# Kernel optimization log

Measured on AMD Instinct MI355X. Metric: run time of the kernel, lower is better.

Reference implementation:

```python
import jax, jax.numpy as jnp
import numpy as np

MAX_WARPING_WINDOW = None  # matches init kwarg (None => full window, no masking)


def _pairwise_euclidean(x, y):
    # x: (B, F, Tx), y: (B, F, Ty) -> (B, Tx, Ty)
    # ||x_t - y_s||_2 computed via the expanded quadratic form (one GEMM instead
    # of materializing the (B, F, Tx, Ty) difference tensor like the torch code).
    x2 = jnp.sum(x * x, axis=1)                      # (B, Tx)
    y2 = jnp.sum(y * y, axis=1)                      # (B, Ty)
    xy = jnp.einsum('bft,bfs->bts', x, y)            # (B, Tx, Ty)
    d2 = jnp.maximum(x2[:, :, None] + y2[:, None, :] - 2.0 * xy, 0.0)
    return jnp.sqrt(d2)


def _dtw(cost):
    # cost: (B, Tx, Ty). Classic DTW DP:
    #   dtw[i, j] = cost[i-1, j-1] + min(dtw[i-1, j], dtw[i, j-1], dtw[i-1, j-1])
    # outer scan over rows i, inner scan over columns j (carries dtw[i, j-1]).
    B, Tx, Ty = cost.shape
    dt = cost.dtype
    INF = jnp.array(jnp.inf, dt)
    cost_t = jnp.transpose(cost, (1, 2, 0))          # (Tx, Ty, B)

    def row_step(carry, cost_row):
        prev_row, left = carry                       # prev_row: (Ty, B) = dtw[i-1, 1:], left: (B,) = dtw[i-1, 0]
        prev_shift = jnp.concatenate([left[None, :], prev_row[:-1]], axis=0)  # dtw[i-1, j-1]
        a = jnp.minimum(prev_row, prev_shift)        # min(dtw[i-1, j], dtw[i-1, j-1])

        def col_step(cur_left, ac):
            a_j, c_j = ac                            # each (B,)
            cur = c_j + jnp.minimum(a_j, cur_left)   # cur_left = dtw[i, j-1]
            return cur, cur

        _, cur_row = jax.lax.scan(col_step, jnp.full((B,), INF, dt), (a, cost_row))
        return (cur_row, jnp.full((B,), INF, dt)), None

    # row 0 of the DP: dtw[0, 0] = 0, dtw[0, j>0] = inf
    init = (jnp.full((Ty, B), INF, dt), jnp.zeros((B,), dt))
    (last_row, _), _ = jax.lax.scan(row_step, init, cost_t)
    return last_row[-1]                              # dtw[Tx, Ty], shape (B,)


def setup_inputs() -> dict:
    key = jax.random.key(0)
    kx, ky = jax.random.split(key)
    B, F, T = 128, 128, 512
    x = jax.random.normal(kx, (B, F, T), dtype=jnp.float32)
    y = jax.random.normal(ky, (B, F, T), dtype=jnp.float32)
    return {"x": x, "y": y}


def reference(x, y):
    cost = _pairwise_euclidean(x, y)                 # (B, Tx, Ty)
    if MAX_WARPING_WINDOW is not None:
        Tx, Ty = cost.shape[1], cost.shape[2]
        p = jnp.arange(Tx)[:, None]
        q = jnp.arange(Ty)[None, :]
        cost = jnp.where(jnp.abs(p - q) <= MAX_WARPING_WINDOW, cost, jnp.inf)
    return _dtw(cost)
```

## Files before the change

kernel.cpp:

```cpp
#include <hip/hip_runtime.h>
#include <stdint.h>

#define B_ 128
#define F_ 128
#define T_ 512
#define TS 64
#define DIAG_N 1024

#define BIGV 1e30f

typedef __attribute__((ext_vector_type(8))) short     bf16x8;
typedef __attribute__((ext_vector_type(4))) float     f32x4;
typedef __attribute__((ext_vector_type(2))) float     f32x2;

static __device__ __forceinline__ unsigned short f32_to_bf16(float f) {
    union { float f; uint32_t u; } v; v.f = f;
    const uint32_t u = v.u + 0x7fffu + ((v.u >> 16) & 1u);
    return (unsigned short)(u >> 16);
}

static __device__ __forceinline__ float wave_shr1(float src, float fill) {
    const int r = __builtin_amdgcn_update_dpp(
        __builtin_bit_cast(int, fill), __builtin_bit_cast(int, src),
        0x138, 0xf, 0xf, false);
    return __builtin_bit_cast(float, r);
}
static __device__ __forceinline__ float wave_shl1(float src, float fill) {
    const int r = __builtin_amdgcn_update_dpp(
        __builtin_bit_cast(int, fill), __builtin_bit_cast(int, src),
        0x130, 0xf, 0xf, false);
    return __builtin_bit_cast(float, r);
}

__global__ __launch_bounds__(256) void dtw_prep_kernel(
    const float* __restrict__ x, const float* __restrict__ y,
    unsigned short* __restrict__ xt, unsigned short* __restrict__ yt,
    float* __restrict__ nx, float* __restrict__ ny)
{
    const int tch = blockIdx.x;
    const int b   = blockIdx.y;
    const int z   = blockIdx.z;
    const int tid = threadIdx.x;
    const int t0  = tch * 64;

    const float* src      = (z == 0 ? x : y) + (size_t)b * F_ * T_;
    unsigned short* dst   = (z == 0 ? xt : yt) + (size_t)b * T_ * F_;
    float* nd             = (z == 0 ? nx : ny) + (size_t)b * T_;

    __shared__ float S[F_][65];

    const int fr = tid >> 4;
    const int q  = (tid & 15) * 4;
#pragma unroll
    for (int p = 0; p < 8; ++p) {
        const int f = p * 16 + fr;
        const float4 v = *(const float4*)(src + (size_t)f * T_ + t0 + q);
        S[f][q] = v.x; S[f][q + 1] = v.y; S[f][q + 2] = v.z; S[f][q + 3] = v.w;
    }
    __syncthreads();

    if (tid < 64) {
        float s = 0.f;
#pragma unroll
        for (int f = 0; f < F_; ++f) { const float v = S[f][tid]; s = fmaf(v, v, s); }
        nd[t0 + tid] = s;
    }

    const int tl = tid >> 2;
    const int fb = (tid & 3) * 32;
    uint32_t pk[16];
#pragma unroll
    for (int e = 0; e < 16; ++e) {
        const uint32_t lo = f32_to_bf16(S[fb + 2 * e][tl]);
        const uint32_t hi = f32_to_bf16(S[fb + 2 * e + 1][tl]);
        pk[e] = lo | (hi << 16);
    }
    uint32_t* o = (uint32_t*)(dst + (size_t)(t0 + tl) * F_ + fb);
#pragma unroll
    for (int e = 0; e < 16; e += 4)
        *(uint4*)(o + e) = make_uint4(pk[e], pk[e + 1], pk[e + 2], pk[e + 3]);
}

__global__ __launch_bounds__(256) void dtw_cost_kernel(
    const unsigned short* __restrict__ xt, const unsigned short* __restrict__ yt,
    const float* __restrict__ nx, const float* __restrict__ ny,
    unsigned char* __restrict__ costD, int b0)
{
    const int tj  = blockIdx.x;
    const int ti  = blockIdx.y;
    const int bl  = blockIdx.z;
    const int b   = b0 + bl;
    const int tid = threadIdx.x;
    const int gi0 = ti * TS;
    const int gj0 = tj * TS;

    const int w    = tid >> 6;
    const int lane = tid & 63;
    const int l15  = lane & 15;
    const int hi   = lane >> 4;

    __shared__ __align__(16) char smem[16384];
    unsigned short* Ys = (unsigned short*)smem;

    {
        const int l16 = tid & 15;
#pragma unroll
        for (int p = 0; p < 4; ++p) {
            const int row = p * 16 + (tid >> 4);
            const uint4 vy = *(const uint4*)(yt + ((size_t)b * T_ + gj0 + row) * F_ + l16 * 8);
            const int byt = (row * 256 + l16 * 16) ^ ((row & 7) << 4);
            *(uint4*)((char*)Ys + byt) = vy;
        }
    }

    const unsigned short* xb = xt + ((size_t)b * T_ + gi0 + 16 * w + l15) * F_ + hi * 8;
    const bf16x8 A0 = *(const bf16x8*)(xb);
    const bf16x8 A1 = *(const bf16x8*)(xb + 32);
    const bf16x8 A2 = *(const bf16x8*)(xb + 64);
    const bf16x8 A3 = *(const bf16x8*)(xb + 96);

    const float4 x2r = *(const float4*)(nx + (size_t)b * T_ + gi0 + 16 * w + 4 * hi);
    float y2c[4];
#pragma unroll
    for (int nt = 0; nt < 4; ++nt)
        y2c[nt] = ny[(size_t)b * T_ + gj0 + nt * 16 + l15];
    const float x2v[4] = {x2r.x, x2r.y, x2r.z, x2r.w};

    __syncthreads();

    f32x4 acc[4] = {};
#pragma unroll
    for (int kb = 0; kb < 4; ++kb) {
        const int koff = kb * 64 + hi * 16;
        const bf16x8 a = (kb == 0) ? A0 : (kb == 1) ? A1 : (kb == 2) ? A2 : A3;
#pragma unroll
        for (int nt = 0; nt < 4; ++nt) {
            const int col = nt * 16 + l15;
            const bf16x8 bb = *(const bf16x8*)((const char*)Ys +
                               ((col * 256 + koff) ^ ((col & 7) << 4)));
            acc[nt] = __builtin_amdgcn_mfma_f32_16x16x32_bf16(a, bb, acc[nt], 0, 0, 0);
        }
    }

    __syncthreads();
    unsigned short* Ts = (unsigned short*)smem;
#pragma unroll
    for (int nt = 0; nt < 4; ++nt) {
        const int col = nt * 16 + l15;
#pragma unroll
        for (int r = 0; r < 4; ++r) {
            const int row = 16 * w + hi * 4 + r;
            const float c = sqrtf(fmaxf(x2v[r] + y2c[nt] - 2.f * acc[nt][r], 0.f));
            const _Float16 hv = (_Float16)c;
            Ts[row * 67 + col] = *(const unsigned short*)&hv;
        }
    }
    __syncthreads();

    unsigned char* outD = costD + (size_t)bl * (DIAG_N * (size_t)T_);
    const int tbase = gi0 + gj0;
#pragma unroll
    for (int q = 0; q < 16; ++q) {
        const int g = q * 4 + w;
        const int d = (lane <= g) ? g : g + 64;
        const _Float16 hval = *(const _Float16*)&Ts[(d - lane) * 67 + lane];
        const float cf = (float)hval;
        const int pk = __builtin_amdgcn_cvt_pk_fp8_f32(cf, cf, 0, false);
        outD[(size_t)(tbase + d) * T_ + gj0 + lane] = (unsigned char)pk;
    }
}

__global__ __launch_bounds__(128, 1) void dtw_dp_bidi(
    const unsigned char* __restrict__ costD, float* __restrict__ out, int b0)
{
    const int bl  = blockIdx.x;
    const int tid = threadIdx.x;
    const int w   = tid >> 6;
    const int L   = tid & 63;
    const unsigned char* gbase = costD + (size_t)bl * (DIAG_N * (size_t)T_) + 16 * L;

    __shared__ __align__(16) unsigned char ringF[32][T_];
    __shared__ __align__(16) unsigned char ringB[32][T_];
    __shared__ __align__(16) float bb2[T_];
    __shared__ __align__(16) float bb3[T_];

    float va0 = BIGV, va1 = BIGV, va2 = BIGV, va3 = BIGV,
          va4 = BIGV, va5 = BIGV, va6 = BIGV, va7 = BIGV;
    float vb0 = BIGV, vb1 = BIGV, vb2 = BIGV, vb3 = BIGV,
          vb4 = BIGV, vb5 = BIGV, vb6 = BIGV, vb7 = BIGV;
    float s2c;
    uint2 ca0, ca1, ca2, ca3, ca4, ca5, ca6, ca7;
    uint2 cb0, cb1, cb2, cb3, cb4, cb5, cb6, cb7;

#define GLDP(RING, row, slot)                                               \
    __builtin_amdgcn_global_load_lds(                                       \
        (const __attribute__((address_space(1))) void*)(gbase + (size_t)(row) * T_), \
        (__attribute__((address_space(3))) void*)(&RING[slot][0]), 16, 0, 0)

#define GLD4F(blk) do {                                                     \
    const int r0_ = (blk) * 8, s0_ = ((blk) & 3) * 8;                       \
    GLDP(ringF, r0_ + 0, s0_ + 0); GLDP(ringF, r0_ + 2, s0_ + 2);           \
    GLDP(ringF, r0_ + 4, s0_ + 4); GLDP(ringF, r0_ + 6, s0_ + 6);           \
} while (0)

#define GLD4B(blk) do {                                                     \
    const int m0_ = 1015 - (blk) * 8, s0_ = ((blk) & 3) * 8;                \
    GLDP(ringB, m0_ + 0, s0_ + 0); GLDP(ringB, m0_ + 2, s0_ + 2);           \
    GLDP(ringB, m0_ + 4, s0_ + 4); GLDP(ringB, m0_ + 6, s0_ + 6);           \
} while (0)

#define WAITV(n)                                                            \
    do { asm volatile("s_waitcnt vmcnt(" #n ")" ::: "memory");              \
         __builtin_amdgcn_sched_barrier(0); } while (0)

#define SB __builtin_amdgcn_sched_barrier(0)

#define RL8(BK, blk) do {                                                   \
    const unsigned char* rp_ = &ringF[((blk) & 3) * 8][8 * L];              \
    BK##0 = *(const uint2*)(rp_ + 0 * T_);                                  \
    BK##1 = *(const uint2*)(rp_ + 1 * T_);                                  \
    BK##2 = *(const uint2*)(rp_ + 2 * T_);                                  \
    BK##3 = *(const uint2*)(rp_ + 3 * T_);                                  \
    BK##4 = *(const uint2*)(rp_ + 4 * T_);                                  \
    BK##5 = *(const uint2*)(rp_ + 5 * T_);                                  \
    BK##6 = *(const uint2*)(rp_ + 6 * T_);                                  \
    BK##7 = *(const uint2*)(rp_ + 7 * T_);                                  \
} while (0)

#define RL8R(BK, blk) do {                                                  \
    const unsigned char* rp_ = &ringB[((blk) & 3) * 8][8 * L];              \
    BK##0 = *(const uint2*)(rp_ + 7 * T_);                                  \
    BK##1 = *(const uint2*)(rp_ + 6 * T_);                                  \
    BK##2 = *(const uint2*)(rp_ + 5 * T_);                                  \
    BK##3 = *(const uint2*)(rp_ + 4 * T_);                                  \
    BK##4 = *(const uint2*)(rp_ + 3 * T_);                                  \
    BK##5 = *(const uint2*)(rp_ + 2 * T_);                                  \
    BK##6 = *(const uint2*)(rp_ + 1 * T_);                                  \
    BK##7 = *(const uint2*)(rp_ + 0 * T_);                                  \
} while (0)

#define CVT8(Hv)                                                            \
    const f32x2 c01 = __builtin_amdgcn_cvt_pk_f32_fp8((int)Hv.x, false);    \
    const f32x2 c23 = __builtin_amdgcn_cvt_pk_f32_fp8((int)Hv.x, true);     \
    const f32x2 c45 = __builtin_amdgcn_cvt_pk_f32_fp8((int)Hv.y, false);    \
    const f32x2 c67 = __builtin_amdgcn_cvt_pk_f32_fp8((int)Hv.y, true)

#define STEPF_A(Hv) do {                                                    \
    const float s1 = wave_shr1(va7, BIGV);                                  \
    CVT8(Hv);                                                               \
    const float n0 = c01[0] + fminf(fminf(va0, s1),  s2c);                  \
    const float n1 = c01[1] + fminf(fminf(va1, va0), vb0);                  \
    const float n2 = c23[0] + fminf(fminf(va2, va1), vb1);                  \
    const float n3 = c23[1] + fminf(fminf(va3, va2), vb2);                  \
    const float n4 = c45[0] + fminf(fminf(va4, va3), vb3);                  \
    const float n5 = c45[1] + fminf(fminf(va5, va4), vb4);                  \
    const float n6 = c67[0] + fminf(fminf(va6, va5), vb5);                  \
    const float n7 = c67[1] + fminf(fminf(va7, va6), vb6);                  \
    s2c = s1;                                                               \
    vb0 = n0; vb1 = n1; vb2 = n2; vb3 = n3;                                 \
    vb4 = n4; vb5 = n5; vb6 = n6; vb7 = n7;                                 \
} while (0)

#define STEPF_B(Hv) do {                                                    \
    const float s1 = wave_shr1(vb7, BIGV);                                  \
    CVT8(Hv);                                                               \
    const float n0 = c01[0] + fminf(fminf(vb0, s1),  s2c);                  \
    const float n1 = c01[1] + fminf(fminf(vb1, vb0), va0);                  \
    const float n2 = c23[0] + fminf(fminf(vb2, vb1), va1);                  \
    const float n3 = c23[1] + fminf(fminf(vb3, vb2), va2);                  \
    const float n4 = c45[0] + fminf(fminf(vb4, vb3), va3);                  \
    const float n5 = c45[1] + fminf(fminf(vb5, vb4), va4);                  \
    const float n6 = c67[0] + fminf(fminf(vb6, vb5), va5);                  \
    const float n7 = c67[1] + fminf(fminf(vb7, vb6), va6);                  \
    s2c = s1;                                                               \
    va0 = n0; va1 = n1; va2 = n2; va3 = n3;                                 \
    va4 = n4; va5 = n5; va6 = n6; va7 = n7;                                 \
} while (0)

#define STEPB_A(Hv) do {                                                    \
    const float s1 = wave_shl1(va0, BIGV);                                  \
    CVT8(Hv);                                                               \
    const float n7 = c67[1] + fminf(fminf(va7, s1),  s2c);                  \
    const float n6 = c67[0] + fminf(fminf(va6, va7), vb7);                  \
    const float n5 = c45[1] + fminf(fminf(va5, va6), vb6);                  \
    const float n4 = c45[0] + fminf(fminf(va4, va5), vb5);                  \
    const float n3 = c23[1] + fminf(fminf(va3, va4), vb4);                  \
    const float n2 = c23[0] + fminf(fminf(va2, va3), vb3);                  \
    const float n1 = c01[1] + fminf(fminf(va1, va2), vb2);                  \
    const float n0 = c01[0] + fminf(fminf(va0, va1), vb1);                  \
    s2c = s1;                                                               \
    vb0 = n0; vb1 = n1; vb2 = n2; vb3 = n3;                                 \
    vb4 = n4; vb5 = n5; vb6 = n6; vb7 = n7;                                 \
} while (0)

#define STEPB_B(Hv) do {                                                    \
    const float s1 = wave_shl1(vb0, BIGV);                                  \
    CVT8(Hv);                                                               \
    const float n7 = c67[1] + fminf(fminf(vb7, s1),  s2c);                  \
    const float n6 = c67[0] + fminf(fminf(vb6, vb7), va7);                  \
    const float n5 = c45[1] + fminf(fminf(vb5, vb6), va6);                  \
    const float n4 = c45[0] + fminf(fminf(vb4, vb5), va5);                  \
    const float n3 = c23[1] + fminf(fminf(vb3, vb4), va4);                  \
    const float n2 = c23[0] + fminf(fminf(vb2, vb3), va3);                  \
    const float n1 = c01[1] + fminf(fminf(vb1, vb2), va2);                  \
    const float n0 = c01[0] + fminf(fminf(vb0, vb1), va1);                  \
    s2c = s1;                                                               \
    va0 = n0; va1 = n1; va2 = n2; va3 = n3;                                 \
    va4 = n4; va5 = n5; va6 = n6; va7 = n7;                                 \
} while (0)

#define STEPF8(BK)                                                          \
    STEPF_A(BK##0); STEPF_B(BK##1); STEPF_A(BK##2); STEPF_B(BK##3);         \
    STEPF_A(BK##4); STEPF_B(BK##5); STEPF_A(BK##6); STEPF_B(BK##7)
#define STEPB8(BK)                                                          \
    STEPB_A(BK##0); STEPB_B(BK##1); STEPB_A(BK##2); STEPB_B(BK##3);         \
    STEPB_A(BK##4); STEPB_B(BK##5); STEPB_A(BK##6); STEPB_B(BK##7)

    if (w == 0) {
        s2c = (L == 0) ? 0.f : BIGV;
        GLD4F(0); GLD4F(1); GLD4F(2); GLD4F(3);
        WAITV(12); RL8(ca, 0); SB;
        int k = 0;
#pragma unroll 1
        for (int it = 0; it < 30; ++it) {
            WAITV(8); RL8(cb, k + 1); SB; STEPF8(ca); SB; GLD4F(k + 4); SB;
            WAITV(8); RL8(ca, k + 2); SB; STEPF8(cb); SB; GLD4F(k + 5); SB;
            k += 2;
        }
        WAITV(8); RL8(cb, 61); SB; STEPF8(ca); SB;
        WAITV(4); RL8(ca, 62); SB; STEPF8(cb); SB;
        WAITV(0); RL8(cb, 63); SB; STEPF8(ca); SB;
        STEPF8(cb);
    } else {
        s2c = (L == 63) ? 0.f : BIGV;
        GLD4B(0); GLD4B(1); GLD4B(2); GLD4B(3);
        WAITV(12); RL8R(ca, 0); SB;
        int k = 0;
#pragma unroll 1
        for (int it = 0; it < 30; ++it) {
            WAITV(8); RL8R(cb, k + 1); SB; STEPB8(ca); SB; GLD4B(k + 4); SB;
            WAITV(8); RL8R(ca, k + 2); SB; STEPB8(cb); SB; GLD4B(k + 5); SB;
            k += 2;
        }
        WAITV(8); RL8R(cb, 61); SB; STEPB8(ca); SB;
        WAITV(4); RL8R(ca, 62); SB; STEPB8(cb); SB;
        WAITV(0); RL8R(cb, 63); SB; STEPB8(ca); SB;
        STEPB_A(cb0); STEPB_B(cb1); STEPB_A(cb2); STEPB_B(cb3);
        STEPB_A(cb4); STEPB_B(cb5); STEPB_A(cb6);
        *(float4*)&bb2[8 * L]     = make_float4(vb0, vb1, vb2, vb3);
        *(float4*)&bb2[8 * L + 4] = make_float4(vb4, vb5, vb6, vb7);
        *(float4*)&bb3[8 * L]     = make_float4(va0, va1, va2, va3);
        *(float4*)&bb3[8 * L + 4] = make_float4(va4, va5, va6, va7);
    }

    __syncthreads();

    if (w == 0) {
        const float4 p0 = *(const float4*)&bb2[8 * L];
        const float4 p1 = *(const float4*)&bb2[8 * L + 4];
        const float4 q0 = *(const float4*)&bb3[8 * L];
        const float4 q1 = *(const float4*)&bb3[8 * L + 4];
        const float b2[8] = {p0.x, p0.y, p0.z, p0.w, p1.x, p1.y, p1.z, p1.w};
        const float b3[8] = {q0.x, q0.y, q0.z, q0.w, q1.x, q1.y, q1.z, q1.w};
        const float F511[8] = {va0, va1, va2, va3, va4, va5, va6, va7};
        const float F510[8] = {vb0, vb1, vb2, vb3, vb4, vb5, vb6, vb7};
        float b2s[8], b3s[8];
#pragma unroll
        for (int kk = 0; kk < 7; ++kk) { b2s[kk] = b2[kk + 1]; b3s[kk] = b3[kk + 1]; }
        b2s[7] = wave_shl1(b2[0], BIGV);
        b3s[7] = wave_shl1(b3[0], BIGV);
        float m = BIGV;
#pragma unroll
        for (int kk = 0; kk < 8; ++kk) {
            const float t1 = F511[kk] + fminf(fminf(b2[kk], b2s[kk]), b3s[kk]);
            const float t2 = F510[kk] + b2s[kk];
            m = fminf(m, fminf(t1, t2));
        }
#pragma unroll
        for (int off = 1; off < 64; off <<= 1)
            m = fminf(m, __shfl_xor(m, off));
        if (L == 0) out[b0 + bl] = m;
    }

#undef GLDP
#undef GLD4F
#undef GLD4B
#undef WAITV
#undef SB
#undef RL8
#undef RL8R
#undef CVT8
#undef STEPF_A
#undef STEPF_B
#undef STEPB_A
#undef STEPB_B
#undef STEPF8
#undef STEPB8
}

extern "C" void kernel_launch(void* const* d_in, const int* in_sizes, int n_in,
                              void* d_out, int out_size, void* d_ws, size_t ws_size,
                              hipStream_t stream)
{
    const float* x = (const float*)d_in[0];
    const float* y = (const float*)d_in[1];
    float* out = (float*)d_out;

    unsigned short* xt = (unsigned short*)d_ws;
    unsigned short* yt = xt + (size_t)B_ * T_ * F_;
    float* nx = (float*)(yt + (size_t)B_ * T_ * F_);
    float* ny = nx + (size_t)B_ * T_;
    unsigned char* costD = (unsigned char*)(ny + (size_t)B_ * T_);
    const size_t head = (size_t)(costD - (unsigned char*)d_ws);

    const size_t perb = (size_t)DIAG_N * T_;
    int Bg = 8;
    for (int g = 128; g >= 8; g >>= 1)
        if (ws_size >= head + perb * (size_t)g) { Bg = g; break; }

    hipLaunchKernelGGL(dtw_prep_kernel, dim3(T_ / 64, B_, 2), dim3(256), 0, stream,
                       x, y, xt, yt, nx, ny);

    for (int b0 = 0; b0 < B_; b0 += Bg) {
        dim3 gc(T_ / TS, T_ / TS, Bg);
        hipLaunchKernelGGL(dtw_cost_kernel, gc, dim3(256), 0, stream,
                           xt, yt, nx, ny, costD, b0);
        hipLaunchKernelGGL(dtw_dp_bidi, dim3(Bg), dim3(128), 0, stream,
                           costD, out, b0);
    }
}
```

Baseline: 97.03 us.

## Interleave two independent batch DTW recurrences per wave in the DP kernel

```diff
diff --git a/kernel.cpp b/kernel.cpp
--- a/kernel.cpp
+++ b/kernel.cpp
@@ -170,43 +170,52 @@
     }
 }
 
-__global__ __launch_bounds__(128, 1) void dtw_dp_bidi(
+__global__ __launch_bounds__(128, 1) void dtw_dp_bidi2(
     const unsigned char* __restrict__ costD, float* __restrict__ out, int b0)
 {
     const int bl  = blockIdx.x;
     const int tid = threadIdx.x;
     const int w   = tid >> 6;
     const int L   = tid & 63;
-    const unsigned char* gbase = costD + (size_t)bl * (DIAG_N * (size_t)T_) + 16 * L;
-
-    __shared__ __align__(16) unsigned char ringF[32][T_];
-    __shared__ __align__(16) unsigned char ringB[32][T_];
-    __shared__ __align__(16) float bb2[T_];
-    __shared__ __align__(16) float bb3[T_];
-
-    float va0 = BIGV, va1 = BIGV, va2 = BIGV, va3 = BIGV,
-          va4 = BIGV, va5 = BIGV, va6 = BIGV, va7 = BIGV;
-    float vb0 = BIGV, vb1 = BIGV, vb2 = BIGV, vb3 = BIGV,
-          vb4 = BIGV, vb5 = BIGV, vb6 = BIGV, vb7 = BIGV;
-    float s2c;
-    uint2 ca0, ca1, ca2, ca3, ca4, ca5, ca6, ca7;
-    uint2 cb0, cb1, cb2, cb3, cb4, cb5, cb6, cb7;
-
-#define GLDP(RING, row, slot)                                               \
+    const unsigned char* gA = costD + (size_t)(2 * bl)     * (DIAG_N * (size_t)T_) + 16 * L;
+    const unsigned char* gB = costD + (size_t)(2 * bl + 1) * (DIAG_N * (size_t)T_) + 16 * L;
+
+    __shared__ __align__(16) unsigned char ringFA[32][T_];
+    __shared__ __align__(16) unsigned char ringFB[32][T_];
+    __shared__ __align__(16) unsigned char ringBA[32][T_];
+    __shared__ __align__(16) unsigned char ringBB[32][T_];
+    __shared__ __align__(16) float bb2[2][T_];
+    __shared__ __align__(16) float bb3[2][T_];
+
+    float Ava0 = BIGV, Ava1 = BIGV, Ava2 = BIGV, Ava3 = BIGV,
+          Ava4 = BIGV, Ava5 = BIGV, Ava6 = BIGV, Ava7 = BIGV;
+    float Avb0 = BIGV, Avb1 = BIGV, Avb2 = BIGV, Avb3 = BIGV,
+          Avb4 = BIGV, Avb5 = BIGV, Avb6 = BIGV, Avb7 = BIGV;
+    float Bva0 = BIGV, Bva1 = BIGV, Bva2 = BIGV, Bva3 = BIGV,
+          Bva4 = BIGV, Bva5 = BIGV, Bva6 = BIGV, Bva7 = BIGV;
+    float Bvb0 = BIGV, Bvb1 = BIGV, Bvb2 = BIGV, Bvb3 = BIGV,
+          Bvb4 = BIGV, Bvb5 = BIGV, Bvb6 = BIGV, Bvb7 = BIGV;
+    float As2c, Bs2c;
+    uint2 Aca0, Aca1, Aca2, Aca3, Aca4, Aca5, Aca6, Aca7;
+    uint2 Acb0, Acb1, Acb2, Acb3, Acb4, Acb5, Acb6, Acb7;
+    uint2 Bca0, Bca1, Bca2, Bca3, Bca4, Bca5, Bca6, Bca7;
+    uint2 Bcb0, Bcb1, Bcb2, Bcb3, Bcb4, Bcb5, Bcb6, Bcb7;
+
+#define GLDP(G, RING, row, slot)                                            \
     __builtin_amdgcn_global_load_lds(                                       \
-        (const __attribute__((address_space(1))) void*)(gbase + (size_t)(row) * T_), \
+        (const __attribute__((address_space(1))) void*)((G) + (size_t)(row) * T_), \
         (__attribute__((address_space(3))) void*)(&RING[slot][0]), 16, 0, 0)
 
-#define GLD4F(blk) do {                                                     \
+#define GLD4F(G, RING, blk) do {                                            \
     const int r0_ = (blk) * 8, s0_ = ((blk) & 3) * 8;                       \
-    GLDP(ringF, r0_ + 0, s0_ + 0); GLDP(ringF, r0_ + 2, s0_ + 2);           \
-    GLDP(ringF, r0_ + 4, s0_ + 4); GLDP(ringF, r0_ + 6, s0_ + 6);           \
-} while (0)
-
-#define GLD4B(blk) do {                                                     \
+    GLDP(G, RING, r0_ + 0, s0_ + 0); GLDP(G, RING, r0_ + 2, s0_ + 2);       \
+    GLDP(G, RING, r0_ + 4, s0_ + 4); GLDP(G, RING, r0_ + 6, s0_ + 6);       \
+} while (0)
+
+#define GLD4B(G, RING, blk) do {                                            \
     const int m0_ = 1015 - (blk) * 8, s0_ = ((blk) & 3) * 8;                \
-    GLDP(ringB, m0_ + 0, s0_ + 0); GLDP(ringB, m0_ + 2, s0_ + 2);           \
-    GLDP(ringB, m0_ + 4, s0_ + 4); GLDP(ringB, m0_ + 6, s0_ + 6);           \
+    GLDP(G, RING, m0_ + 0, s0_ + 0); GLDP(G, RING, m0_ + 2, s0_ + 2);       \
+    GLDP(G, RING, m0_ + 4, s0_ + 4); GLDP(G, RING, m0_ + 6, s0_ + 6);       \
 } while (0)
 
 #define WAITV(n)                                                            \
@@ -215,8 +224,8 @@
 
 #define SB __builtin_amdgcn_sched_barrier(0)
 
-#define RL8(BK, blk) do {                                                   \
-    const unsigned char* rp_ = &ringF[((blk) & 3) * 8][8 * L];              \
+#define RL8(RING, BK, blk) do {                                             \
+    const unsigned char* rp_ = &RING[((blk) & 3) * 8][8 * L];               \
     BK##0 = *(const uint2*)(rp_ + 0 * T_);                                  \
     BK##1 = *(const uint2*)(rp_ + 1 * T_);                                  \
     BK##2 = *(const uint2*)(rp_ + 2 * T_);                                  \
@@ -227,8 +236,8 @@
     BK##7 = *(const uint2*)(rp_ + 7 * T_);                                  \
 } while (0)
 
-#define RL8R(BK, blk) do {                                                  \
-    const unsigned char* rp_ = &ringB[((blk) & 3) * 8][8 * L];              \
+#define RL8R(RING, BK, blk) do {                                            \
+    const unsigned char* rp_ = &RING[((blk) & 3) * 8][8 * L];               \
     BK##0 = *(const uint2*)(rp_ + 7 * T_);                                  \
     BK##1 = *(const uint2*)(rp_ + 6 * T_);                                  \
     BK##2 = *(const uint2*)(rp_ + 5 * T_);                                  \
@@ -245,141 +254,176 @@
     const f32x2 c45 = __builtin_amdgcn_cvt_pk_f32_fp8((int)Hv.y, false);    \
     const f32x2 c67 = __builtin_amdgcn_cvt_pk_f32_fp8((int)Hv.y, true)
 
-#define STEPF_A(Hv) do {                                                    \
-    const float s1 = wave_shr1(va7, BIGV);                                  \
+#define STEPF_A(T, Hv) do {                                                 \
+    const float s1 = wave_shr1(T##va7, BIGV);                               \
     CVT8(Hv);                                                               \
-    const float n0 = c01[0] + fminf(fminf(va0, s1),  s2c);                  \
-    const float n1 = c01[1] + fminf(fminf(va1, va0), vb0);                  \
-    const float n2 = c23[0] + fminf(fminf(va2, va1), vb1);                  \
-    const float n3 = c23[1] + fminf(fminf(va3, va2), vb2);                  \
-    const float n4 = c45[0] + fminf(fminf(va4, va3), vb3);                  \
-    const float n5 = c45[1] + fminf(fminf(va5, va4), vb4);                  \
-    const float n6 = c67[0] + fminf(fminf(va6, va5), vb5);                  \
-    const float n7 = c67[1] + fminf(fminf(va7, va6), vb6);                  \
-    s2c = s1;                                                               \
-    vb0 = n0; vb1 = n1; vb2 = n2; vb3 = n3;                                 \
-    vb4 = n4; vb5 = n5; vb6 = n6; vb7 = n7;                                 \
-} while (0)
-
-#define STEPF_B(Hv) do {                                                    \
-    const float s1 = wave_shr1(vb7, BIGV);                                  \
+    const float n0 = c01[0] + fminf(fminf(T##va0, s1),     T##s2c);         \
+    const float n1 = c01[1] + fminf(fminf(T##va1, T##va0), T##vb0);         \
+    const float n2 = c23[0] + fminf(fminf(T##va2, T##va1), T##vb1);         \
+    const float n3 = c23[1] + fminf(fminf(T##va3, T##va2), T##vb2);         \
+    const float n4 = c45[0] + fminf(fminf(T##va4, T##va3), T##vb3);         \
+    const float n5 = c45[1] + fminf(fminf(T##va5, T##va4), T##vb4);         \
+    const float n6 = c67[0] + fminf(fminf(T##va6, T##va5), T##vb5);         \
+    const float n7 = c67[1] + fminf(fminf(T##va7, T##va6), T##vb6);         \
+    T##s2c = s1;                                                            \
+    T##vb0 = n0; T##vb1 = n1; T##vb2 = n2; T##vb3 = n3;                     \
+    T##vb4 = n4; T##vb5 = n5; T##vb6 = n6; T##vb7 = n7;                     \
+} while (0)
+
+#define STEPF_B(T, Hv) do {                                                 \
+    const float s1 = wave_shr1(T##vb7, BIGV);                               \
     CVT8(Hv);                                                               \
-    const float n0 = c01[0] + fminf(fminf(vb0, s1),  s2c);                  \
-    const float n1 = c01[1] + fminf(fminf(vb1, vb0), va0);                  \
-    const float n2 = c23[0] + fminf(fminf(vb2, vb1), va1);                  \
-    const float n3 = c23[1] + fminf(fminf(vb3, vb2), va2);                  \
-    const float n4 = c45[0] + fminf(fminf(vb4, vb3), va3);                  \
-    const float n5 = c45[1] + fminf(fminf(vb5, vb4), va4);                  \
-    const float n6 = c67[0] + fminf(fminf(vb6, vb5), va5);                  \
-    const float n7 = c67[1] + fminf(fminf(vb7, vb6), va6);                  \
-    s2c = s1;                                                               \
-    va0 = n0; va1 = n1; va2 = n2; va3 = n3;                                 \
-    va4 = n4; va5 = n5; va6 = n6; va7 = n7;                                 \
-} while (0)
-
-#define STEPB_A(Hv) do {                                                    \
-    const float s1 = wave_shl1(va0, BIGV);                                  \
+    const float n0 = c01[0] + fminf(fminf(T##vb0, s1),     T##s2c);         \
+    const float n1 = c01[1] + fminf(fminf(T##vb1, T##vb0), T##va0);         \
+    const float n2 = c23[0] + fminf(fminf(T##vb2, T##vb1), T##va1);         \
+    const float n3 = c23[1] + fminf(fminf(T##vb3, T##vb2), T##va2);         \
+    const float n4 = c45[0] + fminf(fminf(T##vb4, T##vb3), T##va3);         \
+    const float n5 = c45[1] + fminf(fminf(T##vb5, T##vb4), T##va4);         \
+    const float n6 = c67[0] + fminf(fminf(T##vb6, T##vb5), T##va5);         \
+    const float n7 = c67[1] + fminf(fminf(T##vb7, T##vb6), T##va6);         \
+    T##s2c = s1;                                                            \
+    T##va0 = n0; T##va1 = n1; T##va2 = n2; T##va3 = n3;                     \
+    T##va4 = n4; T##va5 = n5; T##va6 = n6; T##va7 = n7;                     \
+} while (0)
+
+#define STEPB_A(T, Hv) do {                                                 \
+    const float s1 = wave_shl1(T##va0, BIGV);                               \
     CVT8(Hv);                                                               \
-    const float n7 = c67[1] + fminf(fminf(va7, s1),  s2c);                  \
-    const float n6 = c67[0] + fminf(fminf(va6, va7), vb7);                  \
-    const float n5 = c45[1] + fminf(fminf(va5, va6), vb6);                  \
-    const float n4 = c45[0] + fminf(fminf(va4, va5), vb5);                  \
-    const float n3 = c23[1] + fminf(fminf(va3, va4), vb4);                  \
-    const float n2 = c23[0] + fminf(fminf(va2, va3), vb3);                  \
-    const float n1 = c01[1] + fminf(fminf(va1, va2), vb2);                  \
-    const float n0 = c01[0] + fminf(fminf(va0, va1), vb1);                  \
-    s2c = s1;                                                               \
-    vb0 = n0; vb1 = n1; vb2 = n2; vb3 = n3;                                 \
-    vb4 = n4; vb5 = n5; vb6 = n6; vb7 = n7;                                 \
-} while (0)
-
-#define STEPB_B(Hv) do {                                                    \
-    const float s1 = wave_shl1(vb0, BIGV);                                  \
+    const float n7 = c67[1] + fminf(fminf(T##va7, s1),     T##s2c);         \
+    const float n6 = c67[0] + fminf(fminf(T##va6, T##va7), T##vb7);         \
+    const float n5 = c45[1] + fminf(fminf(T##va5, T##va6), T##vb6);         \
+    const float n4 = c45[0] + fminf(fminf(T##va4, T##va5), T##vb5);         \
+    const float n3 = c23[1] + fminf(fminf(T##va3, T##va4), T##vb4);         \
+    const float n2 = c23[0] + fminf(fminf(T##va2, T##va3), T##vb3);         \
+    const float n1 = c01[1] + fminf(fminf(T##va1, T##va2), T##vb2);         \
+    const float n0 = c01[0] + fminf(fminf(T##va0, T##va1), T##vb1);         \
+    T##s2c = s1;                                                            \
+    T##vb0 = n0; T##vb1 = n1; T##vb2 = n2; T##vb3 = n3;                     \
+    T##vb4 = n4; T##vb5 = n5; T##vb6 = n6; T##vb7 = n7;                     \
+} while (0)
+
+#define STEPB_B(T, Hv) do {                                                 \
+    const float s1 = wave_shl1(T##vb0, BIGV);                               \
     CVT8(Hv);                                                               \
-    const float n7 = c67[1] + fminf(fminf(vb7, s1),  s2c);                  \
-    const float n6 = c67[0] + fminf(fminf(vb6, vb7), va7);                  \
-    const float n5 = c45[1] + fminf(fminf(vb5, vb6), va6);                  \
-    const float n4 = c45[0] + fminf(fminf(vb4, vb5), va5);                  \
-    const float n3 = c23[1] + fminf(fminf(vb3, vb4), va4);                  \
-    const float n2 = c23[0] + fminf(fminf(vb2, vb3), va3);                  \
-    const float n1 = c01[1] + fminf(fminf(vb1, vb2), va2);                  \
-    const float n0 = c01[0] + fminf(fminf(vb0, vb1), va1);                  \
-    s2c = s1;                                                               \
-    va0 = n0; va1 = n1; va2 = n2; va3 = n3;                                 \
-    va4 = n4; va5 = n5; va6 = n6; va7 = n7;                                 \
-} while (0)
-
-#define STEPF8(BK)                                                          \
-    STEPF_A(BK##0); STEPF_B(BK##1); STEPF_A(BK##2); STEPF_B(BK##3);         \
-    STEPF_A(BK##4); STEPF_B(BK##5); STEPF_A(BK##6); STEPF_B(BK##7)
-#define STEPB8(BK)                                                          \
-    STEPB_A(BK##0); STEPB_B(BK##1); STEPB_A(BK##2); STEPB_B(BK##3);         \
-    STEPB_A(BK##4); STEPB_B(BK##5); STEPB_A(BK##6); STEPB_B(BK##7)
+    const float n7 = c67[1] + fminf(fminf(T##vb7, s1),     T##s2c);         \
+    const float n6 = c67[0] + fminf(fminf(T##vb6, T##vb7), T##va7);         \
+    const float n5 = c45[1] + fminf(fminf(T##vb5, T##vb6), T##va6);         \
+    const float n4 = c45[0] + fminf(fminf(T##vb4, T##vb5), T##va5);         \
+    const float n3 = c23[1] + fminf(fminf(T##vb3, T##vb4), T##va4);         \
+    const float n2 = c23[0] + fminf(fminf(T##vb2, T##vb3), T##va3);         \
+    const float n1 = c01[1] + fminf(fminf(T##vb1, T##vb2), T##va2);         \
+    const float n0 = c01[0] + fminf(fminf(T##vb0, T##vb1), T##va1);         \
+    T##s2c = s1;                                                            \
+    T##va0 = n0; T##va1 = n1; T##va2 = n2; T##va3 = n3;                     \
+    T##va4 = n4; T##va5 = n5; T##va6 = n6; T##va7 = n7;                     \
+} while (0)
+
+#define STEPF8(T, BK)                                                       \
+    STEPF_A(T, BK##0); STEPF_B(T, BK##1); STEPF_A(T, BK##2); STEPF_B(T, BK##3); \
+    STEPF_A(T, BK##4); STEPF_B(T, BK##5); STEPF_A(T, BK##6); STEPF_B(T, BK##7)
+#define STEPB8(T, BK)                                                       \
+    STEPB_A(T, BK##0); STEPB_B(T, BK##1); STEPB_A(T, BK##2); STEPB_B(T, BK##3); \
+    STEPB_A(T, BK##4); STEPB_B(T, BK##5); STEPB_A(T, BK##6); STEPB_B(T, BK##7)
 
     if (w == 0) {
-        s2c = (L == 0) ? 0.f : BIGV;
-        GLD4F(0); GLD4F(1); GLD4F(2); GLD4F(3);
-        WAITV(12); RL8(ca, 0); SB;
+        As2c = (L == 0) ? 0.f : BIGV;
+        Bs2c = (L == 0) ? 0.f : BIGV;
+        GLD4F(gA, ringFA, 0); GLD4F(gB, ringFB, 0);
+        GLD4F(gA, ringFA, 1); GLD4F(gB, ringFB, 1);
+        GLD4F(gA, ringFA, 2); GLD4F(gB, ringFB, 2);
+        GLD4F(gA, ringFA, 3); GLD4F(gB, ringFB, 3);
+        WAITV(24); RL8(ringFA, Aca, 0); RL8(ringFB, Bca, 0); SB;
         int k = 0;
 #pragma unroll 1
         for (int it = 0; it < 30; ++it) {
-            WAITV(8); RL8(cb, k + 1); SB; STEPF8(ca); SB; GLD4F(k + 4); SB;
-            WAITV(8); RL8(ca, k + 2); SB; STEPF8(cb); SB; GLD4F(k + 5); SB;
+            WAITV(16); RL8(ringFA, Acb, k + 1); RL8(ringFB, Bcb, k + 1); SB;
+            STEPF8(A, Aca); STEPF8(B, Bca); SB;
+            GLD4F(gA, ringFA, k + 4); GLD4F(gB, ringFB, k + 4); SB;
+            WAITV(16); RL8(ringFA, Aca, k + 2); RL8(ringFB, Bca, k + 2); SB;
+            STEPF8(A, Acb); STEPF8(B, Bcb); SB;
+            GLD4F(gA, ringFA, k + 5); GLD4F(gB, ringFB, k + 5); SB;
             k += 2;
         }
-        WAITV(8); RL8(cb, 61); SB; STEPF8(ca); SB;
-        WAITV(4); RL8(ca, 62); SB; STEPF8(cb); SB;
-        WAITV(0); RL8(cb, 63); SB; STEPF8(ca); SB;
-        STEPF8(cb);
+        WAITV(16); RL8(ringFA, Acb, 61); RL8(ringFB, Bcb, 61); SB;
+        STEPF8(A, Aca); STEPF8(B, Bca); SB;
+        WAITV(8);  RL8(ringFA, Aca, 62); RL8(ringFB, Bca, 62); SB;
+        STEPF8(A, Acb); STEPF8(B, Bcb); SB;
+        WAITV(0);  RL8(ringFA, Acb, 63); RL8(ringFB, Bcb, 63); SB;
+        STEPF8(A, Aca); STEPF8(B, Bca); SB;
+        STEPF8(A, Acb); STEPF8(B, Bcb);
     } else {
-        s2c = (L == 63) ? 0.f : BIGV;
-        GLD4B(0); GLD4B(1); GLD4B(2); GLD4B(3);
-        WAITV(12); RL8R(ca, 0); SB;
+        As2c = (L == 63) ? 0.f : BIGV;
+        Bs2c = (L == 63) ? 0.f : BIGV;
+        GLD4B(gA, ringBA, 0); GLD4B(gB, ringBB, 0);
+        GLD4B(gA, ringBA, 1); GLD4B(gB, ringBB, 1);
+        GLD4B(gA, ringBA, 2); GLD4B(gB, ringBB, 2);
+        GLD4B(gA, ringBA, 3); GLD4B(gB, ringBB, 3);
+        WAITV(24); RL8R(ringBA, Aca, 0); RL8R(ringBB, Bca, 0); SB;
         int k = 0;
 #pragma unroll 1
         for (int it = 0; it < 30; ++it) {
-            WAITV(8); RL8R(cb, k + 1); SB; STEPB8(ca); SB; GLD4B(k + 4); SB;
-            WAITV(8); RL8R(ca, k + 2); SB; STEPB8(cb); SB; GLD4B(k + 5); SB;
+            WAITV(16); RL8R(ringBA, Acb, k + 1); RL8R(ringBB, Bcb, k + 1); SB;
+            STEPB8(A, Aca); STEPB8(B, Bca); SB;
+            GLD4B(gA, ringBA, k + 4); GLD4B(gB, ringBB, k + 4); SB;
+            WAITV(16); RL8R(ringBA, Aca, k + 2); RL8R(ringBB, Bca, k + 2); SB;
+            STEPB8(A, Acb); STEPB8(B, Bcb); SB;
+            GLD4B(gA, ringBA, k + 5); GLD4B(gB, ringBB, k + 5); SB;
             k += 2;
         }
-        WAITV(8); RL8R(cb, 61); SB; STEPB8(ca); SB;
-        WAITV(4); RL8R(ca, 62); SB; STEPB8(cb); SB;
-        WAITV(0); RL8R(cb, 63); SB; STEPB8(ca); SB;
-        STEPB_A(cb0); STEPB_B(cb1); STEPB_A(cb2); STEPB_B(cb3);
-        STEPB_A(cb4); STEPB_B(cb5); STEPB_A(cb6);
-        *(float4*)&bb2[8 * L]     = make_float4(vb0, vb1, vb2, vb3);
-        *(float4*)&bb2[8 * L + 4] = make_float4(vb4, vb5, vb6, vb7);
-        *(float4*)&bb3[8 * L]     = make_float4(va0, va1, va2, va3);
-        *(float4*)&bb3[8 * L + 4] = make_float4(va4, va5, va6, va7);
+        WAITV(16); RL8R(ringBA, Acb, 61); RL8R(ringBB, Bcb, 61); SB;
+        STEPB8(A, Aca); STEPB8(B, Bca); SB;
+        WAITV(8);  RL8R(ringBA, Aca, 62); RL8R(ringBB, Bca, 62); SB;
+        STEPB8(A, Acb); STEPB8(B, Bcb); SB;
+        WAITV(0);  RL8R(ringBA, Acb, 63); RL8R(ringBB, Bcb, 63); SB;
+        STEPB8(A, Aca); STEPB8(B, Bca); SB;
+        STEPB_A(A, Acb0); STEPB_B(A, Acb1); STEPB_A(A, Acb2); STEPB_B(A, Acb3);
+        STEPB_A(A, Acb4); STEPB_B(A, Acb5); STEPB_A(A, Acb6);
+        STEPB_A(B, Bcb0); STEPB_B(B, Bcb1); STEPB_A(B, Bcb2); STEPB_B(B, Bcb3);
+        STEPB_A(B, Bcb4); STEPB_B(B, Bcb5); STEPB_A(B, Bcb6);
+        *(float4*)&bb2[0][8 * L]     = make_float4(Avb0, Avb1, Avb2, Avb3);
+        *(float4*)&bb2[0][8 * L + 4] = make_float4(Avb4, Avb5, Avb6, Avb7);
+        *(float4*)&bb3[0][8 * L]     = make_float4(Ava0, Ava1, Ava2, Ava3);
+        *(float4*)&bb3[0][8 * L + 4] = make_float4(Ava4, Ava5, Ava6, Ava7);
+        *(float4*)&bb2[1][8 * L]     = make_float4(Bvb0, Bvb1, Bvb2, Bvb3);
+        *(float4*)&bb2[1][8 * L + 4] = make_float4(Bvb4, Bvb5, Bvb6, Bvb7);
+        *(float4*)&bb3[1][8 * L]     = make_float4(Bva0, Bva1, Bva2, Bva3);
+        *(float4*)&bb3[1][8 * L + 4] = make_float4(Bva4, Bva5, Bva6, Bva7);
     }
 
     __syncthreads();
 
     if (w == 0) {
-        const float4 p0 = *(const float4*)&bb2[8 * L];
-        const float4 p1 = *(const float4*)&bb2[8 * L + 4];
-        const float4 q0 = *(const float4*)&bb3[8 * L];
-        const float4 q1 = *(const float4*)&bb3[8 * L + 4];
-        const float b2[8] = {p0.x, p0.y, p0.z, p0.w, p1.x, p1.y, p1.z, p1.w};
-        const float b3[8] = {q0.x, q0.y, q0.z, q0.w, q1.x, q1.y, q1.z, q1.w};
-        const float F511[8] = {va0, va1, va2, va3, va4, va5, va6, va7};
-        const float F510[8] = {vb0, vb1, vb2, vb3, vb4, vb5, vb6, vb7};
-        float b2s[8], b3s[8];
-#pragma unroll
-        for (int kk = 0; kk < 7; ++kk) { b2s[kk] = b2[kk + 1]; b3s[kk] = b3[kk + 1]; }
-        b2s[7] = wave_shl1(b2[0], BIGV);
-        b3s[7] = wave_shl1(b3[0], BIGV);
-        float m = BIGV;
-#pragma unroll
-        for (int kk = 0; kk < 8; ++kk) {
-            const float t1 = F511[kk] + fminf(fminf(b2[kk], b2s[kk]), b3s[kk]);
-            const float t2 = F510[kk] + b2s[kk];
-            m = fminf(m, fminf(t1, t2));
-        }
-#pragma unroll
-        for (int off = 1; off < 64; off <<= 1)
-            m = fminf(m, __shfl_xor(m, off));
-        if (L == 0) out[b0 + bl] = m;
+#define COMBINE(T, qb, outidx) do {                                         \
+        const float4 p0 = *(const float4*)&bb2[qb][8 * L];                  \
+        const float4 p1 = *(const float4*)&bb2[qb][8 * L + 4];              \
+        const float4 q0 = *(const float4*)&bb3[qb][8 * L];                  \
+        const float4 q1 = *(const float4*)&bb3[qb][8 * L + 4];              \
+        const float b2[8] = {p0.x, p0.y, p0.z, p0.w, p1.x, p1.y, p1.z, p1.w}; \
+        const float b3[8] = {q0.x, q0.y, q0.z, q0.w, q1.x, q1.y, q1.z, q1.w}; \
+        const float F511[8] = {T##va0, T##va1, T##va2, T##va3,              \
+                               T##va4, T##va5, T##va6, T##va7};             \
+        const float F510[8] = {T##vb0, T##vb1, T##vb2, T##vb3,              \
+                               T##vb4, T##vb5, T##vb6, T##vb7};             \
+        float b2s[8], b3s[8];                                               \
+        _Pragma("unroll")                                                   \
+        for (int kk = 0; kk < 7; ++kk) { b2s[kk] = b2[kk + 1]; b3s[kk] = b3[kk + 1]; } \
+        b2s[7] = wave_shl1(b2[0], BIGV);                                    \
+        b3s[7] = wave_shl1(b3[0], BIGV);                                    \
+        float m = BIGV;                                                     \
+        _Pragma("unroll")                                                   \
+        for (int kk = 0; kk < 8; ++kk) {                                    \
+            const float t1 = F511[kk] + fminf(fminf(b2[kk], b2s[kk]), b3s[kk]); \
+            const float t2 = F510[kk] + b2s[kk];                            \
+            m = fminf(m, fminf(t1, t2));                                    \
+        }                                                                   \
+        _Pragma("unroll")                                                   \
+        for (int off = 1; off < 64; off <<= 1)                              \
+            m = fminf(m, __shfl_xor(m, off));                               \
+        if (L == 0) out[outidx] = m;                                        \
+} while (0)
+        COMBINE(A, 0, b0 + 2 * bl);
+        COMBINE(B, 1, b0 + 2 * bl + 1);
+#undef COMBINE
     }
 
 #undef GLDP
@@ -425,7 +469,7 @@
         dim3 gc(T_ / TS, T_ / TS, Bg);
         hipLaunchKernelGGL(dtw_cost_kernel, gc, dim3(256), 0, stream,
                            xt, yt, nx, ny, costD, b0);
-        hipLaunchKernelGGL(dtw_dp_bidi, dim3(Bg), dim3(128), 0, stream,
+        hipLaunchKernelGGL(dtw_dp_bidi2, dim3(Bg / 2), dim3(128), 0, stream,
                            costD, out, b0);
     }
 }
```

New measurement: 118.0 us. 21.6% more time.
